# Kernel tuning notes

Measured on AMD Instinct MI355X. Metric: run time of the kernel, lower is better.

## Reference

```python
import jax, jax.numpy as jnp
from jax import lax
import numpy as np

B, CIN, COUT, H, W, K = 4, 64, 64, 128, 128, 3
FACTOR = 2.0  # ivcf, tile != first-layer override path -> factor = ivcf
DN = ('NCHW', 'OIHW', 'NCHW')


def cimu_conv2d(x, weight, bias, factor):
    """Bit-serial int8 conv emulation: 8 bit-plane convs, per-plane clamp/round."""
    xq = jnp.clip(x, -128, 127).astype(jnp.int8).astype(jnp.uint8)  # two's complement bits
    shifts = jnp.arange(8, dtype=jnp.uint8).reshape(8, 1, 1, 1, 1)
    bits = ((xq[None] >> shifts) & jnp.uint8(1)).astype(jnp.float32)  # (8,B,C,Hp,Wp)
    P, b, c, hp, wp = bits.shape
    y = lax.conv_general_dilated(bits.reshape(P * b, c, hp, wp), weight,
                                 window_strides=(1, 1), padding='VALID',
                                 dimension_numbers=DN)  # (8B, Cout, Ho, Wo)
    y = y.reshape(P, b, y.shape[1], y.shape[2], y.shape[3])
    y = jnp.clip(jnp.round(y / factor), -128, 127)
    y = jnp.round(jnp.round(y * factor))
    plane_w = jnp.array([1., 2., 4., 8., 16., 32., 64., -128.], dtype=jnp.float32)
    y = jnp.einsum('pbchw,p->bchw', y, plane_w)
    return y + bias.reshape(1, -1, 1, 1)


def setup_inputs() -> dict:
    key = jax.random.key(0)
    ks = jax.random.split(key, 8)
    ri = lambda k, shape, lo, hi: (jax.random.randint(k, shape, lo, hi)).astype(jnp.float32)
    return {
        'cast_in':   ri(ks[0], (B, CIN, H, W), -128, 128),
        'merge_in':  ri(ks[1], (B, COUT, H, W), -128, 128),
        'gather_in': ri(ks[2], (B, COUT, H, W), -128, 128),
        'conv_weight': ri(ks[3], (COUT, CIN, K, K), -3, 4),
        'conv_bias':   ri(ks[4], (COUT,), -8, 8),
        'ctrans_i': ri(ks[5], (COUT,), 1, 4),            # per-channel integer multiplier
        'ctrans_s': jnp.full((COUT,), -1.0, jnp.float32),  # per-channel shift exponent
        'strans_i': jnp.float32(3.0),
        'strans_s': jnp.float32(-2.0),
        'atrans_i': jnp.float32(1.0),
        'atrans_s': jnp.float32(0.0),
    }


def reference(cast_in, merge_in, gather_in, conv_weight, conv_bias,
              ctrans_i, ctrans_s, strans_i, strans_s, atrans_i, atrans_s):
    # conv_pads = [1,1,1,1] (left,right,top,bottom on last two dims)
    x = jnp.pad(cast_in, ((0, 0), (0, 0), (1, 1), (1, 1)))
    x = cimu_conv2d(x, conv_weight, conv_bias, FACTOR)
    # merge add
    x = x + merge_in
    # merge-node quantize (hardtrans): mult = ctrans_i / 2^{-ctrans_s}
    cmult = (ctrans_i / (2.0 ** (-ctrans_s))).reshape(1, -1, 1, 1)
    x = jnp.clip(jnp.round(x * cmult), -128, 127)
    # gather add + quantize
    x = x + gather_in
    smult = strans_i / (2.0 ** (-strans_s))
    x = jnp.clip(jnp.round(x * smult), -128, 127)
    # Relu + quantize
    x = jax.nn.relu(x)
    amult = atrans_i / (2.0 ** (-atrans_s))
    x = jnp.clip(jnp.round(x * amult), -128, 127)
    # pool_pads = [0,0,0,0] (no-op), MaxPool 2x2 stride 2
    x = lax.reduce_window(x, -jnp.inf, lax.max, (1, 1, 2, 2), (1, 1, 2, 2), 'VALID')
    return x
```

## Files before the change

kernel.cpp:

```cpp
#include <hip/hip_runtime.h>
#include <cstdint>


typedef int i32x4  __attribute__((ext_vector_type(4)));
typedef int i32x16 __attribute__((ext_vector_type(16)));

#define XB_OFF   0u
#define XB_BYTES 4326400u
#define MG_OFF   (XB_OFF + XB_BYTES)
#define MG_BYTES 4194304u
#define GT_OFF   (MG_OFF + MG_BYTES)
#define WPK_OFF  (GT_OFF + MG_BYTES)
#define WPK_BYTES 36864u

__global__ __launch_bounds__(256) void k_stage(const float* __restrict__ s_cast,
                                               const float* __restrict__ s_mg,
                                               const float* __restrict__ s_gt,
                                               const float* __restrict__ wsrc,
                                               uint8_t* __restrict__ ws) {
  const int blk = blockIdx.x, t = threadIdx.x;
  if (blk >= 1680) {
    const int hb = blk - 1680;
    const int b = hb >> 1, r = (hb & 1) ? 129 : 0;
    uint8_t* base = ws + XB_OFF + ((size_t)(b * 130 + r) * 130) * 64;
    const uint4 z = {0, 0, 0, 0};
#pragma unroll
    for (int i = 0; i < 3; ++i) {
      const int s = i * 256 + t;
      if (s < 520) *(uint4*)(base + (size_t)s * 16) = z;
    }
    return;
  }
  if (blk >= 1536) {
    const int idx = (blk - 1536) * 256 + t;
    const int i = idx & 15, l = (idx >> 4) & 63, gg = (idx >> 10) & 1,
              c = idx >> 11;
    const int k = c * 32 + (l >> 5) * 16 + i;
    const int tap = k >> 6, ci = k & 63;
    const int kh = tap / 3, kw = tap % 3;
    const int cco = gg * 32 + (l & 31);
    const float wv = wsrc[((cco * 64 + ci) * 3 + kh) * 3 + kw];
    ((int8_t*)(ws + WPK_OFF))[idx] = (int8_t)(int)wv;
    return;
  }
  const int which = blk >> 9, rem = blk & 511;
  const float* src = which == 0 ? s_cast : (which == 1 ? s_mg : s_gt);
  uint8_t* dst = which == 0 ? (ws + XB_OFF)
                            : (which == 1 ? (ws + MG_OFF) : (ws + GT_OFF));
  const int b = rem >> 7, h = rem & 127;
  __shared__ uint8_t lds[128 * 68];
  const float* s0 = src + ((size_t)(b * 64) * 128 + h) * 128;
#pragma unroll
  for (int ci0 = 0; ci0 < 64; ci0 += 2) {
    const int ci = ci0 + (t >> 7), w = t & 127;
    const float v = s0[ci * 16384 + w];
    lds[w * 68 + ci] = (uint8_t)((int)v & 0xFF);
  }
  __syncthreads();
  if (which == 0) {
    uint8_t* row = dst + (((size_t)b * 130 + h + 1) * 130) * 64;
#pragma unroll
    for (int j = 0; j < 8; ++j) {
      const int f = j * 256 + t;
      const int w = f >> 4, ci4 = f & 15;
      const uint32_t val = *(const uint32_t*)&lds[w * 68 + ci4 * 4];
      *(uint32_t*)(row + 64 + (size_t)f * 4) = val;
    }
    if (t < 8) {
      const int col = (t < 4) ? 0 : 129, seg = t & 3;
      const uint4 z = {0, 0, 0, 0};
      *(uint4*)(row + (size_t)col * 64 + seg * 16) = z;
    }
  } else {
    uint8_t* d0 = dst + ((size_t)(b * 128 + h) * 128) * 64;
#pragma unroll
    for (int j = 0; j < 8; ++j) {
      const int f = j * 256 + t;
      const int w = f >> 4, ci4 = f & 15;
      const uint32_t val = *(const uint32_t*)&lds[w * 68 + ci4 * 4];
      *(uint32_t*)(d0 + (size_t)f * 4) = val;
    }
  }
}

__global__ __launch_bounds__(256, 2) void k_main(
    const unsigned char* __restrict__ xb, const signed char* __restrict__ mg,
    const signed char* __restrict__ gt, const int8_t* __restrict__ wpk,
    const float* __restrict__ bias, const float* __restrict__ cti,
    const float* __restrict__ cts, const float* __restrict__ sti,
    const float* __restrict__ sts, const float* __restrict__ ati,
    const float* __restrict__ ats, float* __restrict__ outp) {
  const int tid = threadIdx.x, lane = tid & 63, wv = tid >> 6;
  const int blk = blockIdx.x;
  const int wq = blk & 3, ho = (blk >> 2) & 63, b = blk >> 8;
  const int h = ho * 2, w0 = wq * 32;

  __shared__ uint4 ldsx4[640];
  __shared__ float po_lds[16 * 64];
  uint8_t* ldsx = (uint8_t*)ldsx4;

  {
    const unsigned char* xrow = xb + ((size_t)(b * 130 + h) * 130 + w0) * 64;
#pragma unroll
    for (int i = 0; i < 3; ++i) {
      const int s = i * 256 + tid;
      if (s < 640) {
        const int row = s / 160, rm = s - row * 160;
        const int col = rm >> 2, ci16 = rm & 3;
        const int gcol = col < 34 ? col : 33;
        const uint4 v =
            *(const uint4*)(xrow + ((size_t)row * 130 + gcol) * 64 + ci16 * 16);
        *(uint4*)(ldsx + (row * 40 + col) * 64 + ci16 * 16) = v;
      }
    }
  }

  i32x4 Bf[36];
#pragma unroll
  for (int cg = 0; cg < 36; ++cg)
    Bf[cg] = *(const i32x4*)(wpk + ((size_t)cg * 64 + lane) * 16);

  const int pix = (lane & 31) >> 3;
  const int plane = lane & 7;
  const int khalf = lane >> 5;
  const int dh = pix >> 1, dw = pix & 1;
  const uint8_t* lbase0 = ldsx + (dh * 40 + dw) * 64 + khalf * 16;

  const int col = lane & 31;
  const float bs0 = bias[col], bs1 = bias[col + 32];
  const float cm0 = ldexpf(cti[col], (int)cts[col]);
  const float cm1 = ldexpf(cti[col + 32], (int)cts[col + 32]);
  const float sm = ldexpf(sti[0], (int)sts[0]);
  const float am = ldexpf(ati[0], (int)ats[0]);
  float pwl[4];
  pwl[0] = khalf ? 16.f : 1.f;
  pwl[1] = khalf ? 32.f : 2.f;
  pwl[2] = khalf ? 64.f : 4.f;
  pwl[3] = khalf ? -128.f : 8.f;

  __syncthreads();

  for (int q = 0; q < 4; ++q) {
    const int wol = wv * 4 + q;
    const int w = (wq * 16 + wol) * 2;
    const uint8_t* lb = lbase0 + wol * 128;

    int mgv[8], gtv[8];
#pragma unroll
    for (int px = 0; px < 4; ++px) {
      const size_t moff =
          ((size_t)((b * 128 + h + (px >> 1)) * 128 + w + (px & 1))) * 64 + col;
      mgv[px] = mg[moff];
      gtv[px] = gt[moff];
      mgv[4 + px] = mg[moff + 32];
      gtv[4 + px] = gt[moff + 32];
    }

#define XOFF(c) ((((c) >> 1) / 3) * 2560 + (((c) >> 1) % 3) * 64 + ((c)&1) * 32)
    uint4 p0 = *(const uint4*)(lb + XOFF(0));
    uint4 p1 = *(const uint4*)(lb + XOFF(1));
    uint4 p2 = *(const uint4*)(lb + XOFF(2));
    i32x16 a0 = {}, a1 = {};
#pragma unroll
    for (int c = 0; c < 18; ++c) {
      uint4 cur;
      if (c % 3 == 0) cur = p0;
      else if (c % 3 == 1) cur = p1;
      else cur = p2;
      if (c + 3 < 18) {
        const uint4 nv = *(const uint4*)(lb + XOFF(c + 3));
        if (c % 3 == 0) p0 = nv;
        else if (c % 3 == 1) p1 = nv;
        else p2 = nv;
      }
      i32x4 av;
      av[0] = (int)((cur.x >> plane) & 0x01010101u);
      av[1] = (int)((cur.y >> plane) & 0x01010101u);
      av[2] = (int)((cur.z >> plane) & 0x01010101u);
      av[3] = (int)((cur.w >> plane) & 0x01010101u);
      a0 = __builtin_amdgcn_mfma_i32_32x32x32_i8(av, Bf[c * 2 + 0], a0, 0, 0, 0);
      a1 = __builtin_amdgcn_mfma_i32_32x32x32_i8(av, Bf[c * 2 + 1], a1, 0, 0, 0);
    }
#undef XOFF

#pragma unroll
    for (int gg = 0; gg < 2; ++gg) {
      const i32x16& acc = gg ? a1 : a0;
      const float bs = gg ? bs1 : bs0;
      const float cm = gg ? cm1 : cm0;
      float psum[4];
#pragma unroll
      for (int px = 0; px < 4; ++px) {
        float s = 0.f;
#pragma unroll
        for (int j = 0; j < 4; ++j) {
          const float y = (float)acc[px * 4 + j];
          const float qq = fminf(fmaxf(rintf(y * 0.5f), -128.f), 127.f);
          s = fmaf(pwl[j], 2.f * qq, s);
        }
        psum[px] = s;
      }
#pragma unroll
      for (int px = 0; px < 4; ++px)
        psum[px] += __shfl_xor(psum[px], 32);

      float po = -3.0e38f;
#pragma unroll
      for (int px = 0; px < 4; ++px) {
        const float x1 = psum[px] + bs + (float)mgv[gg * 4 + px];
        const float x2 = fminf(fmaxf(rintf(x1 * cm), -128.f), 127.f);
        const float x3 = x2 + (float)gtv[gg * 4 + px];
        const float x4 = fminf(fmaxf(rintf(x3 * sm), -128.f), 127.f);
        const float x5 = fmaxf(x4, 0.f);
        const float x6 = fminf(fmaxf(rintf(x5 * am), -128.f), 127.f);
        po = fmaxf(po, x6);
      }
      if (lane < 32)
        po_lds[wol * 64 + gg * 32 + col] = po;
    }
  }

  __syncthreads();
  {
    const int tco = tid >> 2, seg = tid & 3;
    float4 v;
    v.x = po_lds[(seg * 4 + 0) * 64 + tco];
    v.y = po_lds[(seg * 4 + 1) * 64 + tco];
    v.z = po_lds[(seg * 4 + 2) * 64 + tco];
    v.w = po_lds[(seg * 4 + 3) * 64 + tco];
    float* dst = outp + (((size_t)(b * 64 + tco)) * 64 + ho) * 64 + wq * 16 + seg * 4;
    *(float4*)dst = v;
  }
}

extern "C" void kernel_launch(void* const* d_in, const int* in_sizes, int n_in,
                              void* d_out, int out_size, void* d_ws, size_t ws_size,
                              hipStream_t stream) {
  const float* cast_in = (const float*)d_in[0];
  const float* merge_in = (const float*)d_in[1];
  const float* gather_in = (const float*)d_in[2];
  const float* conv_w = (const float*)d_in[3];
  const float* conv_b = (const float*)d_in[4];
  const float* cti = (const float*)d_in[5];
  const float* cts = (const float*)d_in[6];
  const float* sti = (const float*)d_in[7];
  const float* sts = (const float*)d_in[8];
  const float* ati = (const float*)d_in[9];
  const float* ats = (const float*)d_in[10];

  uint8_t* ws = (uint8_t*)d_ws;
  uint8_t* xb = ws + XB_OFF;
  int8_t* mg = (int8_t*)(ws + MG_OFF);
  int8_t* gt = (int8_t*)(ws + GT_OFF);
  int8_t* wpk = (int8_t*)(ws + WPK_OFF);

  k_stage<<<1688, 256, 0, stream>>>(cast_in, merge_in, gather_in, conv_w, ws);
  k_main<<<1024, 256, 0, stream>>>(xb, mg, gt, wpk, conv_b, cti, cts, sti, sts,
                                   ati, ats, (float*)d_out);
}
```

Measured before the change: 40.51 us.

## Read merge and gather inputs directly as fp32 in main kernel via LDS

Drops the staging pass that converted merge_in and gather_in to NHWC int8 in the workspace. The main kernel now loads the needed fp32 tiles directly with float4 loads and transposes them through a padded shared-memory buffer. This removes one write and one read of two 4MB int8 buffers plus the extra staging blocks. In exchange it adds roughly 33KB of LDS per block, which may lower occupancy, and the main kernel now reads the larger fp32 data.

```diff
diff --git a/kernel.cpp b/kernel.cpp
--- a/kernel.cpp
+++ b/kernel.cpp
@@ -7,20 +7,15 @@
 
 #define XB_OFF   0u
 #define XB_BYTES 4326400u
-#define MG_OFF   (XB_OFF + XB_BYTES)
-#define MG_BYTES 4194304u
-#define GT_OFF   (MG_OFF + MG_BYTES)
-#define WPK_OFF  (GT_OFF + MG_BYTES)
+#define WPK_OFF  XB_BYTES
 #define WPK_BYTES 36864u
 
 __global__ __launch_bounds__(256) void k_stage(const float* __restrict__ s_cast,
-                                               const float* __restrict__ s_mg,
-                                               const float* __restrict__ s_gt,
                                                const float* __restrict__ wsrc,
                                                uint8_t* __restrict__ ws) {
   const int blk = blockIdx.x, t = threadIdx.x;
-  if (blk >= 1680) {
-    const int hb = blk - 1680;
+  if (blk >= 656) {
+    const int hb = blk - 656;
     const int b = hb >> 1, r = (hb & 1) ? 129 : 0;
     uint8_t* base = ws + XB_OFF + ((size_t)(b * 130 + r) * 130) * 64;
     const uint4 z = {0, 0, 0, 0};
@@ -31,8 +26,8 @@
     }
     return;
   }
-  if (blk >= 1536) {
-    const int idx = (blk - 1536) * 256 + t;
+  if (blk >= 512) {
+    const int idx = (blk - 512) * 256 + t;
     const int i = idx & 15, l = (idx >> 4) & 63, gg = (idx >> 10) & 1,
               c = idx >> 11;
     const int k = c * 32 + (l >> 5) * 16 + i;
@@ -43,13 +38,9 @@
     ((int8_t*)(ws + WPK_OFF))[idx] = (int8_t)(int)wv;
     return;
   }
-  const int which = blk >> 9, rem = blk & 511;
-  const float* src = which == 0 ? s_cast : (which == 1 ? s_mg : s_gt);
-  uint8_t* dst = which == 0 ? (ws + XB_OFF)
-                            : (which == 1 ? (ws + MG_OFF) : (ws + GT_OFF));
-  const int b = rem >> 7, h = rem & 127;
+  const int b = blk >> 7, h = blk & 127;
   __shared__ uint8_t lds[128 * 68];
-  const float* s0 = src + ((size_t)(b * 64) * 128 + h) * 128;
+  const float* s0 = s_cast + ((size_t)(b * 64) * 128 + h) * 128;
 #pragma unroll
   for (int ci0 = 0; ci0 < 64; ci0 += 2) {
     const int ci = ci0 + (t >> 7), w = t & 127;
@@ -57,35 +48,24 @@
     lds[w * 68 + ci] = (uint8_t)((int)v & 0xFF);
   }
   __syncthreads();
-  if (which == 0) {
-    uint8_t* row = dst + (((size_t)b * 130 + h + 1) * 130) * 64;
-#pragma unroll
-    for (int j = 0; j < 8; ++j) {
-      const int f = j * 256 + t;
-      const int w = f >> 4, ci4 = f & 15;
-      const uint32_t val = *(const uint32_t*)&lds[w * 68 + ci4 * 4];
-      *(uint32_t*)(row + 64 + (size_t)f * 4) = val;
-    }
-    if (t < 8) {
-      const int col = (t < 4) ? 0 : 129, seg = t & 3;
-      const uint4 z = {0, 0, 0, 0};
-      *(uint4*)(row + (size_t)col * 64 + seg * 16) = z;
-    }
-  } else {
-    uint8_t* d0 = dst + ((size_t)(b * 128 + h) * 128) * 64;
-#pragma unroll
-    for (int j = 0; j < 8; ++j) {
-      const int f = j * 256 + t;
-      const int w = f >> 4, ci4 = f & 15;
-      const uint32_t val = *(const uint32_t*)&lds[w * 68 + ci4 * 4];
-      *(uint32_t*)(d0 + (size_t)f * 4) = val;
-    }
+  uint8_t* row = ws + XB_OFF + (((size_t)b * 130 + h + 1) * 130) * 64;
+#pragma unroll
+  for (int j = 0; j < 8; ++j) {
+    const int f = j * 256 + t;
+    const int w = f >> 4, ci4 = f & 15;
+    const uint32_t val = *(const uint32_t*)&lds[w * 68 + ci4 * 4];
+    *(uint32_t*)(row + 64 + (size_t)f * 4) = val;
+  }
+  if (t < 8) {
+    const int col = (t < 4) ? 0 : 129, seg = t & 3;
+    const uint4 z = {0, 0, 0, 0};
+    *(uint4*)(row + (size_t)col * 64 + seg * 16) = z;
   }
 }
 
 __global__ __launch_bounds__(256, 2) void k_main(
-    const unsigned char* __restrict__ xb, const signed char* __restrict__ mg,
-    const signed char* __restrict__ gt, const int8_t* __restrict__ wpk,
+    const unsigned char* __restrict__ xb, const float* __restrict__ mgf,
+    const float* __restrict__ gtf, const int8_t* __restrict__ wpk,
     const float* __restrict__ bias, const float* __restrict__ cti,
     const float* __restrict__ cts, const float* __restrict__ sti,
     const float* __restrict__ sts, const float* __restrict__ ati,
@@ -96,6 +76,7 @@
   const int h = ho * 2, w0 = wq * 32;
 
   __shared__ uint4 ldsx4[640];
+  __shared__ float mgt[2][2][32][65];
   __shared__ float po_lds[16 * 64];
   uint8_t* ldsx = (uint8_t*)ldsx4;
 
@@ -112,6 +93,20 @@
             *(const uint4*)(xrow + ((size_t)row * 130 + gcol) * 64 + ci16 * 16);
         *(uint4*)(ldsx + (row * 40 + col) * 64 + ci16 * 16) = v;
       }
+    }
+  }
+
+#pragma unroll
+  for (int which = 0; which < 2; ++which) {
+    const float* sp = which ? gtf : mgf;
+#pragma unroll
+    for (int i = 0; i < 4; ++i) {
+      const int slot = i * 256 + tid;
+      const int co = slot >> 4, r = slot & 15, hh = r & 1, seg = r >> 1;
+      const float4 v = *(const float4*)(
+          sp + ((size_t)((b * 64 + co) * 128 + h + hh)) * 128 + w0 + seg * 4);
+      float* dst = &mgt[which][hh][seg * 4][co];
+      dst[0] = v.x; dst[65] = v.y; dst[130] = v.z; dst[195] = v.w;
     }
   }
 
@@ -142,19 +137,7 @@
 
   for (int q = 0; q < 4; ++q) {
     const int wol = wv * 4 + q;
-    const int w = (wq * 16 + wol) * 2;
     const uint8_t* lb = lbase0 + wol * 128;
-
-    int mgv[8], gtv[8];
-#pragma unroll
-    for (int px = 0; px < 4; ++px) {
-      const size_t moff =
-          ((size_t)((b * 128 + h + (px >> 1)) * 128 + w + (px & 1))) * 64 + col;
-      mgv[px] = mg[moff];
-      gtv[px] = gt[moff];
-      mgv[4 + px] = mg[moff + 32];
-      gtv[4 + px] = gt[moff + 32];
-    }
 
 #define XOFF(c) ((((c) >> 1) / 3) * 2560 + (((c) >> 1) % 3) * 64 + ((c)&1) * 32)
     uint4 p0 = *(const uint4*)(lb + XOFF(0));
@@ -188,6 +171,7 @@
       const i32x16& acc = gg ? a1 : a0;
       const float bs = gg ? bs1 : bs0;
       const float cm = gg ? cm1 : cm0;
+      const int cc = gg * 32 + col;
       float psum[4];
 #pragma unroll
       for (int px = 0; px < 4; ++px) {
@@ -207,9 +191,10 @@
       float po = -3.0e38f;
 #pragma unroll
       for (int px = 0; px < 4; ++px) {
-        const float x1 = psum[px] + bs + (float)mgv[gg * 4 + px];
+        const int ww = wol * 2 + (px & 1);
+        const float x1 = psum[px] + bs + mgt[0][px >> 1][ww][cc];
         const float x2 = fminf(fmaxf(rintf(x1 * cm), -128.f), 127.f);
-        const float x3 = x2 + (float)gtv[gg * 4 + px];
+        const float x3 = x2 + mgt[1][px >> 1][ww][cc];
         const float x4 = fminf(fmaxf(rintf(x3 * sm), -128.f), 127.f);
         const float x5 = fmaxf(x4, 0.f);
         const float x6 = fminf(fmaxf(rintf(x5 * am), -128.f), 127.f);
@@ -250,11 +235,9 @@
 
   uint8_t* ws = (uint8_t*)d_ws;
   uint8_t* xb = ws + XB_OFF;
-  int8_t* mg = (int8_t*)(ws + MG_OFF);
-  int8_t* gt = (int8_t*)(ws + GT_OFF);
   int8_t* wpk = (int8_t*)(ws + WPK_OFF);
 
-  k_stage<<<1688, 256, 0, stream>>>(cast_in, merge_in, gather_in, conv_w, ws);
-  k_main<<<1024, 256, 0, stream>>>(xb, mg, gt, wpk, conv_b, cti, cts, sti, sts,
-                                   ati, ats, (float*)d_out);
+  k_stage<<<664, 256, 0, stream>>>(cast_in, conv_w, ws);
+  k_main<<<1024, 256, 0, stream>>>(xb, merge_in, gather_in, wpk, conv_b, cti,
+                                   cts, sti, sts, ati, ats, (float*)d_out);
 }
```

Measured after the change: 35.40 us. -12.6%, faster.
